# Kernel tuning notes

Measured on AMD Instinct MI355X. Metric: run time of the kernel, lower is better.

The kernel has to match this reference:

```python
import jax, jax.numpy as jnp
import numpy as np
import math

# ---- irreps config: (multiplicity, l); parity implied by the fixed path list ----
IRREPS_IN = [(32, 0), (32, 1)]    # "32x0e + 32x1o" -> dim 128
IRREPS_SH = [(1, 0), (1, 1), (1, 2)]  # "1x0e + 1x1o + 1x2e" -> dim 9
IRREPS_OUT = [(32, 0), (32, 1)]   # dim 128
# parity/triangle-allowed 'uvw' instructions: (in_block, sh_block, out_block)
PATHS = [(0, 0, 0), (0, 1, 1), (1, 0, 1), (1, 1, 0), (1, 2, 1)]
NUM_NODES = 50000
NUM_EDGES = 800000


def _fact(n):
    return math.factorial(int(round(n)))


def _su2_cg(j1, j2, j3):
    """SU(2) Clebsch-Gordan coefficients via the Racah formula."""
    C = np.zeros((2 * j1 + 1, 2 * j2 + 1, 2 * j3 + 1))
    for m1 in range(-j1, j1 + 1):
        for m2 in range(-j2, j2 + 1):
            m3 = m1 + m2
            if abs(m3) > j3:
                continue
            vmin = int(max(-j1 + j2 + m3, -j1 + m1, 0))
            vmax = int(min(j2 + j3 + m1, j3 - j1 + j2, j3 + m3))
            c = math.sqrt((2 * j3 + 1) * _fact(j3 + j1 - j2) * _fact(j3 - j1 + j2)
                          * _fact(j1 + j2 - j3) / _fact(j1 + j2 + j3 + 1))
            c *= math.sqrt(_fact(j3 + m3) * _fact(j3 - m3) * _fact(j1 - m1)
                           * _fact(j1 + m1) * _fact(j2 - m2) * _fact(j2 + m2))
            s = 0.0
            for v in range(vmin, vmax + 1):
                s += ((-1.0) ** (v + j2 + m2) * _fact(j2 + j3 + m1 - v) * _fact(j1 - m1 + v)
                      / (_fact(v) * _fact(j3 - j1 + j2 - v) * _fact(j3 + m3 - v) * _fact(v + j1 - j2 - m3)))
            C[j1 + m1, j2 + m2, j3 + m3] = c * s
    return C


def _q(l):
    """Change of basis real -> complex spherical harmonics (e3nn convention)."""
    q = np.zeros((2 * l + 1, 2 * l + 1), dtype=np.complex128)
    for m in range(-l, 0):
        q[l + m, l + abs(m)] = 1.0 / np.sqrt(2.0)
        q[l + m, l - abs(m)] = -1j / np.sqrt(2.0)
    q[l, l] = 1.0
    for m in range(1, l + 1):
        q[l + m, l + abs(m)] = (-1.0) ** m / np.sqrt(2.0)
        q[l + m, l - abs(m)] = 1j * (-1.0) ** m / np.sqrt(2.0)
    return (-1j) ** l * q


def _real_cg(l1, l2, l3):
    """Real (Wigner-3j-like) Clebsch-Gordan tensor, unit Frobenius norm."""
    C = _su2_cg(l1, l2, l3).astype(np.complex128)
    C = np.einsum('ij,kl,mn,ikn->jlm', _q(l1), _q(l2), np.conj(_q(l3).T), C)
    C = np.real(C)
    return (C / np.linalg.norm(C)).astype(np.float32)


CG = [jnp.asarray(_real_cg(IRREPS_IN[i1][1], IRREPS_SH[i2][1], IRREPS_OUT[io][1]))
      for (i1, i2, io) in PATHS]
N_PATHS_TO_OUT = {io: sum(1 for p in PATHS if p[2] == io) for io in range(len(IRREPS_OUT))}


def _split(x, irreps):
    """Split flat irreps vector into [E, mul, 2l+1] blocks."""
    blocks, off = [], 0
    for mul, l in irreps:
        d = mul * (2 * l + 1)
        blocks.append(x[:, off:off + d].reshape(x.shape[0], mul, 2 * l + 1))
        off += d
    return blocks


def setup_inputs() -> dict:
    key = jax.random.key(0)
    k1, k2, k3, k4 = jax.random.split(key, 4)
    in_dim = sum(m * (2 * l + 1) for m, l in IRREPS_IN)
    sh_dim = sum(m * (2 * l + 1) for m, l in IRREPS_SH)
    features = jax.random.normal(k1, (NUM_NODES, in_dim), dtype=jnp.float32)
    edge_sh = jax.random.normal(k2, (NUM_EDGES, sh_dim), dtype=jnp.float32)
    edge_index = jax.random.randint(k3, (2, NUM_EDGES), 0, NUM_NODES, dtype=jnp.int32)
    # shared 'uvw' weights: one [mul_in=32, mul_out=32] matrix per path (mul_sh=1)
    weights = jax.random.normal(k4, (len(PATHS), 32, 32), dtype=jnp.float32)
    return {"features": features, "edge_sh": edge_sh,
            "edge_index": edge_index, "weights": weights}


def reference(features, edge_sh, edge_index, weights):
    src, dst = edge_index[0], edge_index[1]
    x1 = _split(features[src], IRREPS_IN)   # gather source node features per edge
    x2 = _split(edge_sh, IRREPS_SH)
    out_blocks = [None] * len(IRREPS_OUT)
    for p, (i1, i2, io) in enumerate(PATHS):
        u, v = IRREPS_IN[i1][0], IRREPS_SH[i2][0]
        alpha = 1.0 / math.sqrt(u * v * N_PATHS_TO_OUT[io])
        # tmp: [E, u, 2*l3+1]; sh block has mul 1 -> squeeze
        tmp = jnp.einsum('eui,ej,ijk->euk', x1[i1], x2[i2][:, 0, :], CG[p])
        msg = jnp.einsum('euk,uw->ewk', tmp, weights[p]) * alpha
        out_blocks[io] = msg if out_blocks[io] is None else out_blocks[io] + msg
    E = edge_sh.shape[0]
    msgs = jnp.concatenate([b.reshape(E, -1) for b in out_blocks], axis=1)  # [E, 128]
    out = jnp.zeros((features.shape[0], msgs.shape[1]), dtype=features.dtype)
    return out.at[dst].add(msgs)  # scatter-add to destination nodes
```

## Files before the change

### kernel.cpp

```cpp
#include <hip/hip_runtime.h>
#include <math.h>


typedef __attribute__((ext_vector_type(8))) short bf16x8;
typedef __attribute__((ext_vector_type(4))) float f32x4;

__device__ inline float blo(unsigned u) { return __uint_as_float(u << 16); }
__device__ inline float bhi(unsigned u) { return __uint_as_float(u & 0xffff0000u); }
__device__ inline unsigned bpack(float a, float b) {
    unsigned ua = __float_as_uint(a);
    ua = (ua + 0x7fffu + ((ua >> 16) & 1u)) >> 16;
    unsigned ub = __float_as_uint(b);
    ub = (ub + 0x7fffu + ((ub >> 16) & 1u)) & 0xffff0000u;
    return ua | ub;
}
__device__ inline unsigned short bh(float a) {
    unsigned ua = __float_as_uint(a);
    return (unsigned short)((ua + 0x7fffu + ((ua >> 16) & 1u)) >> 16);
}

__device__ inline float dfactf(int n) {
    float r = 1.0f;
    for (int i = 2; i <= n; ++i) r *= (float)i;
    return r;
}

__device__ float su2_cg_elem_f(int l1, int l2, int l3, int i, int k, int n) {
    int m1 = i - l1, m2 = k - l2, m3 = n - l3;
    if (m1 + m2 != m3) return 0.0f;
    int vmin = -l1 + l2 + m3;
    if (-l1 + m1 > vmin) vmin = -l1 + m1;
    if (0 > vmin) vmin = 0;
    int vmax = l2 + l3 + m1;
    if (l3 - l1 + l2 < vmax) vmax = l3 - l1 + l2;
    if (l3 + m3 < vmax) vmax = l3 + m3;
    if (vmax < vmin) return 0.0f;
    float c = sqrtf((float)(2 * l3 + 1) * dfactf(l3 + l1 - l2) *
                    dfactf(l3 - l1 + l2) * dfactf(l1 + l2 - l3) /
                    dfactf(l1 + l2 + l3 + 1));
    c *= sqrtf(dfactf(l3 + m3) * dfactf(l3 - m3) * dfactf(l1 - m1) *
               dfactf(l1 + m1) * dfactf(l2 - m2) * dfactf(l2 + m2));
    float s = 0.0f;
    for (int v = vmin; v <= vmax; ++v) {
        float term = dfactf(l2 + l3 + m1 - v) * dfactf(l1 - m1 + v) /
                     (dfactf(v) * dfactf(l3 - l1 + l2 - v) *
                      dfactf(l3 + m3 - v) * dfactf(v + l1 - l2 - m3));
        if ((v + l2 + m2) & 1) term = -term;
        s += term;
    }
    return c * s;
}

__device__ void cg_compute_block(float* __restrict__ cg_out) {
    __shared__ float sqr[3][5][5], sqi[3][5][5];
    __shared__ float vals[5][45];
    int t = threadIdx.x;
    if (t < 75) {
        int l = t / 25, a = (t % 25) / 5, b = t % 5;
        float re = 0.f, im = 0.f;
        const float inv = 0.70710678118654752440f;
        int m = a - l;
        if (a < 5 && b < 5) {
            if (m < 0) {
                if (b == l - m) re = inv;
                if (b == l + m) im = -inv;
            } else if (m == 0) {
                if (b == l && a == l) re = 1.f;
            } else {
                float sgn = (m & 1) ? -1.f : 1.f;
                if (b == l + m) re = sgn * inv;
                if (b == l - m) im = sgn * inv;
            }
        }
        if (l == 1) { float r = re; re = im; im = -r; }
        else if (l == 2) { re = -re; im = -im; }
        sqr[l][a][b] = re;
        sqi[l][a][b] = im;
    }
    __syncthreads();
    const int l1s[5] = {0, 0, 1, 1, 1};
    const int l2s[5] = {0, 1, 0, 1, 2};
    const int l3s[5] = {0, 1, 1, 0, 1};
    const int offs[5] = {0, 1, 10, 19, 28};
    const float alphas[5] = {0.125f, 0.10206207261596575f, 0.10206207261596575f,
                             0.125f, 0.10206207261596575f};
    int p = t / 45, idx = t % 45;
    bool active = (t < 225);
    float acc = 0.0f;
    int d1 = 0, d2 = 0, d3 = 0;
    int l1 = 0, l2 = 0, l3 = 0;
    if (active) {
        l1 = l1s[p]; l2 = l2s[p]; l3 = l3s[p];
        d1 = 2 * l1 + 1; d2 = 2 * l2 + 1; d3 = 2 * l3 + 1;
        if (idx < d1 * d2 * d3) {
            int j = idx / (d2 * d3);
            int rem = idx % (d2 * d3);
            int l_ = rem / d3, m = rem % d3;
            for (int i = 0; i < d1; ++i)
                for (int k = 0; k < d2; ++k)
                    for (int n = 0; n < d3; ++n) {
                        float C = su2_cg_elem_f(l1, l2, l3, i, k, n);
                        if (C == 0.0f) continue;
                        float ar = sqr[l1][i][j], ai = sqi[l1][i][j];
                        float br = sqr[l2][k][l_], bi = sqi[l2][k][l_];
                        float cr = sqr[l3][n][m], ci = sqi[l3][n][m];
                        float abr = ar * br - ai * bi;
                        float abi = ar * bi + ai * br;
                        acc += (abr * cr + abi * ci) * C;
                    }
        }
        vals[p][idx] = acc;
    }
    __syncthreads();
    if (active && idx < d1 * d2 * d3) {
        float n2 = 0.0f;
        for (int q = 0; q < 45; ++q) n2 += vals[p][q] * vals[p][q];
        cg_out[offs[p] + idx] = acc * alphas[p] / sqrtf(n2);
    }
}

__global__ __launch_bounds__(256) void prep_kernel(
    const float* __restrict__ feat, const int* __restrict__ eidx,
    int* __restrict__ cursor, unsigned* __restrict__ fb,
    float* __restrict__ cg, int N, int E) {
    if (blockIdx.x == 0) cg_compute_block(cg);
    int t = blockIdx.x * 256 + threadIdx.x;
    if (t < N * 32) {
        int n = t >> 5, u = t & 31;
        const float* f = feat + (size_t)n * 128;
        float s = f[u];
        float vx = f[32 + 3 * u], vy = f[33 + 3 * u], vz = f[34 + 3 * u];
        ((uint2*)fb)[t] = make_uint2(bpack(s, vx), bpack(vy, vz));
    }
    if (t < E) atomicAdd(&cursor[eidx[E + t]], 1);
}

__global__ __launch_bounds__(256) void scanA_kernel(
    const int* __restrict__ counts, int* __restrict__ tilesums, int N,
    const float* __restrict__ W, const float* __restrict__ cg,
    unsigned short* __restrict__ WBT) {
    __shared__ int lds[4];
    int i = blockIdx.x * 256 + threadIdx.x;
    int v = (i < N) ? counts[i] : 0;
#pragma unroll
    for (int d = 1; d < 64; d <<= 1) v += __shfl_xor(v, d);
    int wid = threadIdx.x >> 6;
    if ((threadIdx.x & 63) == 0) lds[wid] = v;
    __syncthreads();
    if (threadIdx.x == 0)
        tilesums[blockIdx.x] = lds[0] + lds[1] + lds[2] + lds[3];
    int idx = i;
    if (idx < 128 * 352) {
        int j = idx / 352, k = idx % 352;
        int t = k >> 5, u = k & 31;
        float val = 0.f;
        if (j < 32) {
            if (t == 0) val = cg[0] * W[u * 32 + j];
            else if (t == 1) val = W[3072 + u * 32 + j];
        } else {
            int w = (j - 32) / 3, m = (j - 32) % 3;
            if (t >= 2 && t <= 4) { if (t - 2 == m) val = W[1024 + u * 32 + w]; }
            else if (t >= 5 && t <= 7) { val = cg[10 + (t - 5) * 3 + m] * W[2048 + u * 32 + w]; }
            else if (t >= 8) { if (t - 8 == m) val = W[4096 + u * 32 + w]; }
        }
        WBT[idx] = bh(val);
    }
}

__global__ __launch_bounds__(256) void scanB_kernel(
    int* __restrict__ tilesums, int tiles) {
    __shared__ int lds[4];
    int tid = threadIdx.x;
    int v = (tid < tiles) ? tilesums[tid] : 0;
    int orig = v;
#pragma unroll
    for (int d = 1; d < 64; d <<= 1) {
        int t = __shfl_up(v, d);
        if ((tid & 63) >= d) v += t;
    }
    int wid = tid >> 6;
    if ((tid & 63) == 63) lds[wid] = v;
    __syncthreads();
    int base = 0;
    for (int q = 0; q < wid; ++q) base += lds[q];
    if (tid < tiles) tilesums[tid] = base + v - orig;
}

__global__ __launch_bounds__(256) void scanC_kernel(
    int* __restrict__ counts, const int* __restrict__ tilesums, int N) {
    __shared__ int lds[4];
    int i = blockIdx.x * 256 + threadIdx.x;
    int tid = threadIdx.x;
    int v = (i < N) ? counts[i] : 0;
    int orig = v;
#pragma unroll
    for (int d = 1; d < 64; d <<= 1) {
        int t = __shfl_up(v, d);
        if ((tid & 63) >= d) v += t;
    }
    int wid = tid >> 6;
    if ((tid & 63) == 63) lds[wid] = v;
    __syncthreads();
    int base = tilesums[blockIdx.x];
    for (int q = 0; q < wid; ++q) base += lds[q];
    if (i < N) counts[i] = base + v - orig;
}

__global__ __launch_bounds__(256) void zscatter_kernel(
    const int* __restrict__ eidx, const float* __restrict__ sh,
    const float* __restrict__ cg, int* __restrict__ cursor,
    unsigned* __restrict__ zrec, int E) {
    int t = blockIdx.x * 256 + threadIdx.x;
    if (t >= E) return;
    int src = eidx[t];
    int dst = eidx[E + t];
    int pos = atomicAdd(&cursor[dst], 1);
    const float* Ye = sh + (size_t)t * 9;
    float Y0 = Ye[0];
    float Y1v[3] = {Ye[1], Ye[2], Ye[3]};
    float Y2v[5] = {Ye[4], Ye[5], Ye[6], Ye[7], Ye[8]};
    float Z1[3], Z3[3], Z4[9];
#pragma unroll
    for (int m = 0; m < 3; ++m)
        Z1[m] = fmaf(Y1v[0], cg[1 + m],
                fmaf(Y1v[1], cg[4 + m], Y1v[2] * cg[7 + m]));
#pragma unroll
    for (int i = 0; i < 3; ++i)
        Z3[i] = fmaf(Y1v[0], cg[19 + i * 3],
                fmaf(Y1v[1], cg[19 + i * 3 + 1], Y1v[2] * cg[19 + i * 3 + 2]));
#pragma unroll
    for (int i = 0; i < 3; ++i)
#pragma unroll
        for (int m = 0; m < 3; ++m) {
            float acc = 0.f;
#pragma unroll
            for (int j = 0; j < 5; ++j)
                acc = fmaf(Y2v[j], cg[28 + (i * 5 + j) * 3 + m], acc);
            Z4[i * 3 + m] = acc;
        }
    uint2* rec = (uint2*)(zrec + (size_t)pos * 10);
    rec[0] = make_uint2((unsigned)src, bpack(Y0, Z1[0]));
    rec[1] = make_uint2(bpack(Z1[1], Z1[2]), bpack(Z3[0], Z3[1]));
    rec[2] = make_uint2(bpack(Z3[2], Z4[0]), bpack(Z4[1], Z4[2]));
    rec[3] = make_uint2(bpack(Z4[3], Z4[4]), bpack(Z4[5], Z4[6]));
    rec[4] = make_uint2(bpack(Z4[7], Z4[8]), 0u);
}

__global__ __launch_bounds__(256) void gather_kernel(
    const unsigned* __restrict__ fb, const unsigned* __restrict__ zrec,
    const int* __restrict__ cursor, unsigned short* __restrict__ G, int N) {
    int wave = (blockIdx.x * 256 + threadIdx.x) >> 6;
    int lane = threadIdx.x & 63;
    if (wave >= N) return;
    int start = wave ? cursor[wave - 1] : 0;
    int end = cursor[wave];
    int half = lane >> 5, u = lane & 31;

    float g0 = 0.f, g3 = 0.f;
    float g1x = 0.f, g1y = 0.f, g1z = 0.f;
    float g2x = 0.f, g2y = 0.f, g2z = 0.f;
    float g4x = 0.f, g4y = 0.f, g4z = 0.f;

    for (int idx = start + half; idx < end; idx += 2) {
        const uint2* r = (const uint2*)(zrec + (size_t)idx * 10);
        uint2 r0 = r[0], r1 = r[1], r2 = r[2], r3 = r[3], r4 = r[4];
        int src = (int)r0.x;
        uint2 f2 = ((const uint2*)fb)[(size_t)src * 32 + u];
        float s = blo(f2.x), vx = bhi(f2.x);
        float vy = blo(f2.y), vz = bhi(f2.y);
        float y0 = blo(r0.y), z10 = bhi(r0.y);
        float z11 = blo(r1.x), z12 = bhi(r1.x);
        float z30 = blo(r1.y), z31 = bhi(r1.y);
        float z32 = blo(r2.x), z400 = bhi(r2.x);
        float z401 = blo(r2.y), z402 = bhi(r2.y);
        float z410 = blo(r3.x), z411 = bhi(r3.x);
        float z412 = blo(r3.y), z420 = bhi(r3.y);
        float z421 = blo(r4.x), z422 = bhi(r4.x);

        g0 = fmaf(y0, s, g0);
        g1x = fmaf(z10, s, g1x); g1y = fmaf(z11, s, g1y); g1z = fmaf(z12, s, g1z);
        g2x = fmaf(y0, vx, g2x); g2y = fmaf(y0, vy, g2y); g2z = fmaf(y0, vz, g2z);
        g3 = fmaf(z30, vx, fmaf(z31, vy, fmaf(z32, vz, g3)));
        g4x = fmaf(vx, z400, fmaf(vy, z410, fmaf(vz, z420, g4x)));
        g4y = fmaf(vx, z401, fmaf(vy, z411, fmaf(vz, z421, g4y)));
        g4z = fmaf(vx, z402, fmaf(vy, z412, fmaf(vz, z422, g4z)));
    }
    g0 += __shfl_xor(g0, 32);  g3 += __shfl_xor(g3, 32);
    g1x += __shfl_xor(g1x, 32); g1y += __shfl_xor(g1y, 32); g1z += __shfl_xor(g1z, 32);
    g2x += __shfl_xor(g2x, 32); g2y += __shfl_xor(g2y, 32); g2z += __shfl_xor(g2z, 32);
    g4x += __shfl_xor(g4x, 32); g4y += __shfl_xor(g4y, 32); g4z += __shfl_xor(g4z, 32);

    if (half == 0) {
        unsigned short* Gr = G + (size_t)wave * 352 + u;
        Gr[0] = bh(g0);
        Gr[32] = bh(g3);
        Gr[64] = bh(g1x);  Gr[96] = bh(g1y);  Gr[128] = bh(g1z);
        Gr[160] = bh(g2x); Gr[192] = bh(g2y); Gr[224] = bh(g2z);
        Gr[256] = bh(g4x); Gr[288] = bh(g4y); Gr[320] = bh(g4z);
    }
}

__global__ __launch_bounds__(256) void epilogue_kernel(
    const unsigned short* __restrict__ G, const unsigned short* __restrict__ WBT,
    float* __restrict__ out, int N) {
    int wid = (blockIdx.x * 256 + threadIdx.x) >> 6;
    int lane = threadIdx.x & 63;
    int ntiles = N >> 4;
    if (wid >= ntiles) return;
    int n0 = wid << 4;
    int r = lane & 15, q = lane >> 4;

    bf16x8 a[11];
#pragma unroll
    for (int kk = 0; kk < 11; ++kk)
        a[kk] = *(const bf16x8*)(G + (size_t)(n0 + r) * 352 + kk * 32 + q * 8);

#pragma unroll
    for (int jt = 0; jt < 8; ++jt) {
        f32x4 acc = {0.f, 0.f, 0.f, 0.f};
#pragma unroll
        for (int kk = 0; kk < 11; ++kk) {
            bf16x8 b = *(const bf16x8*)(WBT + (size_t)(jt * 16 + r) * 352 + kk * 32 + q * 8);
            acc = __builtin_amdgcn_mfma_f32_16x16x32_bf16(a[kk], b, acc, 0, 0, 0);
        }
#pragma unroll
        for (int i = 0; i < 4; ++i)
            out[(size_t)(n0 + q * 4 + i) * 128 + jt * 16 + r] = acc[i];
    }
}

extern "C" void kernel_launch(void* const* d_in, const int* in_sizes, int n_in,
                              void* d_out, int out_size, void* d_ws, size_t ws_size,
                              hipStream_t stream) {
    const float* feat = (const float*)d_in[0];
    const float* sh = (const float*)d_in[1];
    const int* eidx = (const int*)d_in[2];
    const float* W = (const float*)d_in[3];
    float* out = (float*)d_out;
    int N = in_sizes[0] / 128;
    int E = in_sizes[1] / 9;

    float* wsf = (float*)d_ws;
    float* cg = wsf;
    int* cursor = (int*)(wsf + 128);
    size_t off = (size_t)(128 + N + 1) & ~(size_t)1;
    unsigned* zrec = (unsigned*)(wsf + off);
    unsigned* fb = zrec + (size_t)10 * E;
    unsigned short* G = (unsigned short*)(fb + (size_t)64 * N);
    unsigned short* WBT = G + (size_t)352 * N;
    int* tilesums = (int*)(WBT + 45056);

    int tiles = (N + 255) / 256;

    hipMemsetAsync(cursor, 0, (size_t)N * sizeof(int), stream);
    prep_kernel<<<(N * 32 + 255) / 256, 256, 0, stream>>>(feat, eidx, cursor, fb, cg, N, E);
    scanA_kernel<<<tiles, 256, 0, stream>>>(cursor, tilesums, N, W, cg, WBT);
    scanB_kernel<<<1, 256, 0, stream>>>(tilesums, tiles);
    scanC_kernel<<<tiles, 256, 0, stream>>>(cursor, tilesums, N);
    zscatter_kernel<<<(E + 255) / 256, 256, 0, stream>>>(eidx, sh, cg, cursor, zrec, E);
    gather_kernel<<<(N * 64 + 255) / 256, 256, 0, stream>>>(fb, zrec, cursor, G, N);
    epilogue_kernel<<<((N >> 4) * 64 + 255) / 256, 256, 0, stream>>>(G, WBT, out, N);
}
```

Baseline: 186.0 us.

## Fuse gather and MFMA epilogue kernels via shared-memory G tile

Merges the per-node gather kernel and the MFMA epilogue into one kernel. Each block gathers 16 nodes, four per wave, into a shared-memory bf16 tile, then runs the 16x352x128 MFMA product, with each wave producing two of the eight output column tiles. This removes the global round trip of the G buffer and one kernel launch. In exchange each wave processes four nodes serially and there is a block-wide barrier, which cuts parallelism and latency hiding in the gather phase.

```diff
diff --git a/kernel.cpp b/kernel.cpp
--- a/kernel.cpp
+++ b/kernel.cpp
@@ -88,9 +88,8 @@
     bool active = (t < 225);
     float acc = 0.0f;
     int d1 = 0, d2 = 0, d3 = 0;
-    int l1 = 0, l2 = 0, l3 = 0;
     if (active) {
-        l1 = l1s[p]; l2 = l2s[p]; l3 = l3s[p];
+        int l1 = l1s[p], l2 = l2s[p], l3 = l3s[p];
         d1 = 2 * l1 + 1; d2 = 2 * l2 + 1; d3 = 2 * l3 + 1;
         if (idx < d1 * d2 * d3) {
             int j = idx / (d2 * d3);
@@ -246,77 +245,78 @@
     rec[4] = make_uint2(bpack(Z4[7], Z4[8]), 0u);
 }
 
-__global__ __launch_bounds__(256) void gather_kernel(
+__global__ __launch_bounds__(256) void gather_mfma_kernel(
     const unsigned* __restrict__ fb, const unsigned* __restrict__ zrec,
-    const int* __restrict__ cursor, unsigned short* __restrict__ G, int N) {
-    int wave = (blockIdx.x * 256 + threadIdx.x) >> 6;
+    const int* __restrict__ cursor, const unsigned short* __restrict__ WBT,
+    float* __restrict__ out, int N) {
+    __shared__ unsigned short Gs[16][360];
+    int wv = threadIdx.x >> 6;
     int lane = threadIdx.x & 63;
-    if (wave >= N) return;
-    int start = wave ? cursor[wave - 1] : 0;
-    int end = cursor[wave];
     int half = lane >> 5, u = lane & 31;
-
-    float g0 = 0.f, g3 = 0.f;
-    float g1x = 0.f, g1y = 0.f, g1z = 0.f;
-    float g2x = 0.f, g2y = 0.f, g2z = 0.f;
-    float g4x = 0.f, g4y = 0.f, g4z = 0.f;
-
-    for (int idx = start + half; idx < end; idx += 2) {
-        const uint2* r = (const uint2*)(zrec + (size_t)idx * 10);
-        uint2 r0 = r[0], r1 = r[1], r2 = r[2], r3 = r[3], r4 = r[4];
-        int src = (int)r0.x;
-        uint2 f2 = ((const uint2*)fb)[(size_t)src * 32 + u];
-        float s = blo(f2.x), vx = bhi(f2.x);
-        float vy = blo(f2.y), vz = bhi(f2.y);
-        float y0 = blo(r0.y), z10 = bhi(r0.y);
-        float z11 = blo(r1.x), z12 = bhi(r1.x);
-        float z30 = blo(r1.y), z31 = bhi(r1.y);
-        float z32 = blo(r2.x), z400 = bhi(r2.x);
-        float z401 = blo(r2.y), z402 = bhi(r2.y);
-        float z410 = blo(r3.x), z411 = bhi(r3.x);
-        float z412 = blo(r3.y), z420 = bhi(r3.y);
-        float z421 = blo(r4.x), z422 = bhi(r4.x);
-
-        g0 = fmaf(y0, s, g0);
-        g1x = fmaf(z10, s, g1x); g1y = fmaf(z11, s, g1y); g1z = fmaf(z12, s, g1z);
-        g2x = fmaf(y0, vx, g2x); g2y = fmaf(y0, vy, g2y); g2z = fmaf(y0, vz, g2z);
-        g3 = fmaf(z30, vx, fmaf(z31, vy, fmaf(z32, vz, g3)));
-        g4x = fmaf(vx, z400, fmaf(vy, z410, fmaf(vz, z420, g4x)));
-        g4y = fmaf(vx, z401, fmaf(vy, z411, fmaf(vz, z421, g4y)));
-        g4z = fmaf(vx, z402, fmaf(vy, z412, fmaf(vz, z422, g4z)));
-    }
-    g0 += __shfl_xor(g0, 32);  g3 += __shfl_xor(g3, 32);
-    g1x += __shfl_xor(g1x, 32); g1y += __shfl_xor(g1y, 32); g1z += __shfl_xor(g1z, 32);
-    g2x += __shfl_xor(g2x, 32); g2y += __shfl_xor(g2y, 32); g2z += __shfl_xor(g2z, 32);
-    g4x += __shfl_xor(g4x, 32); g4y += __shfl_xor(g4y, 32); g4z += __shfl_xor(g4z, 32);
-
-    if (half == 0) {
-        unsigned short* Gr = G + (size_t)wave * 352 + u;
-        Gr[0] = bh(g0);
-        Gr[32] = bh(g3);
-        Gr[64] = bh(g1x);  Gr[96] = bh(g1y);  Gr[128] = bh(g1z);
-        Gr[160] = bh(g2x); Gr[192] = bh(g2y); Gr[224] = bh(g2z);
-        Gr[256] = bh(g4x); Gr[288] = bh(g4y); Gr[320] = bh(g4z);
-    }
-}
-
-__global__ __launch_bounds__(256) void epilogue_kernel(
-    const unsigned short* __restrict__ G, const unsigned short* __restrict__ WBT,
-    float* __restrict__ out, int N) {
-    int wid = (blockIdx.x * 256 + threadIdx.x) >> 6;
-    int lane = threadIdx.x & 63;
-    int ntiles = N >> 4;
-    if (wid >= ntiles) return;
-    int n0 = wid << 4;
+    int base = blockIdx.x << 4;
+
+#pragma unroll 1
+    for (int d = 0; d < 4; ++d) {
+        int row = wv * 4 + d;
+        int node = base + row;
+        if (node >= N) break;
+        int start = node ? cursor[node - 1] : 0;
+        int end = cursor[node];
+
+        float g0 = 0.f, g3 = 0.f;
+        float g1x = 0.f, g1y = 0.f, g1z = 0.f;
+        float g2x = 0.f, g2y = 0.f, g2z = 0.f;
+        float g4x = 0.f, g4y = 0.f, g4z = 0.f;
+
+        for (int idx = start + half; idx < end; idx += 2) {
+            const uint2* r = (const uint2*)(zrec + (size_t)idx * 10);
+            uint2 r0 = r[0], r1 = r[1], r2 = r[2], r3 = r[3], r4 = r[4];
+            int src = (int)r0.x;
+            uint2 f2 = ((const uint2*)fb)[(size_t)src * 32 + u];
+            float s = blo(f2.x), vx = bhi(f2.x);
+            float vy = blo(f2.y), vz = bhi(f2.y);
+            float y0 = blo(r0.y), z10 = bhi(r0.y);
+            float z11 = blo(r1.x), z12 = bhi(r1.x);
+            float z30 = blo(r1.y), z31 = bhi(r1.y);
+            float z32 = blo(r2.x), z400 = bhi(r2.x);
+            float z401 = blo(r2.y), z402 = bhi(r2.y);
+            float z410 = blo(r3.x), z411 = bhi(r3.x);
+            float z412 = blo(r3.y), z420 = bhi(r3.y);
+            float z421 = blo(r4.x), z422 = bhi(r4.x);
+
+            g0 = fmaf(y0, s, g0);
+            g1x = fmaf(z10, s, g1x); g1y = fmaf(z11, s, g1y); g1z = fmaf(z12, s, g1z);
+            g2x = fmaf(y0, vx, g2x); g2y = fmaf(y0, vy, g2y); g2z = fmaf(y0, vz, g2z);
+            g3 = fmaf(z30, vx, fmaf(z31, vy, fmaf(z32, vz, g3)));
+            g4x = fmaf(vx, z400, fmaf(vy, z410, fmaf(vz, z420, g4x)));
+            g4y = fmaf(vx, z401, fmaf(vy, z411, fmaf(vz, z421, g4y)));
+            g4z = fmaf(vx, z402, fmaf(vy, z412, fmaf(vz, z422, g4z)));
+        }
+        g0 += __shfl_xor(g0, 32);  g3 += __shfl_xor(g3, 32);
+        g1x += __shfl_xor(g1x, 32); g1y += __shfl_xor(g1y, 32); g1z += __shfl_xor(g1z, 32);
+        g2x += __shfl_xor(g2x, 32); g2y += __shfl_xor(g2y, 32); g2z += __shfl_xor(g2z, 32);
+        g4x += __shfl_xor(g4x, 32); g4y += __shfl_xor(g4y, 32); g4z += __shfl_xor(g4z, 32);
+
+        if (half == 0) {
+            unsigned short* Gr = &Gs[row][u];
+            Gr[0] = bh(g0);
+            Gr[32] = bh(g3);
+            Gr[64] = bh(g1x);  Gr[96] = bh(g1y);  Gr[128] = bh(g1z);
+            Gr[160] = bh(g2x); Gr[192] = bh(g2y); Gr[224] = bh(g2z);
+            Gr[256] = bh(g4x); Gr[288] = bh(g4y); Gr[320] = bh(g4z);
+        }
+    }
+    __syncthreads();
+
     int r = lane & 15, q = lane >> 4;
-
     bf16x8 a[11];
 #pragma unroll
     for (int kk = 0; kk < 11; ++kk)
-        a[kk] = *(const bf16x8*)(G + (size_t)(n0 + r) * 352 + kk * 32 + q * 8);
-
-#pragma unroll
-    for (int jt = 0; jt < 8; ++jt) {
+        a[kk] = *(const bf16x8*)(&Gs[r][kk * 32 + q * 8]);
+
+#pragma unroll
+    for (int jj = 0; jj < 2; ++jj) {
+        int jt = wv * 2 + jj;
         f32x4 acc = {0.f, 0.f, 0.f, 0.f};
 #pragma unroll
         for (int kk = 0; kk < 11; ++kk) {
@@ -324,8 +324,10 @@
             acc = __builtin_amdgcn_mfma_f32_16x16x32_bf16(a[kk], b, acc, 0, 0, 0);
         }
 #pragma unroll
-        for (int i = 0; i < 4; ++i)
-            out[(size_t)(n0 + q * 4 + i) * 128 + jt * 16 + r] = acc[i];
+        for (int i = 0; i < 4; ++i) {
+            int n = base + q * 4 + i;
+            if (n < N) out[(size_t)n * 128 + jt * 16 + r] = acc[i];
+        }
     }
 }
 
@@ -346,11 +348,11 @@
     size_t off = (size_t)(128 + N + 1) & ~(size_t)1;
     unsigned* zrec = (unsigned*)(wsf + off);
     unsigned* fb = zrec + (size_t)10 * E;
-    unsigned short* G = (unsigned short*)(fb + (size_t)64 * N);
-    unsigned short* WBT = G + (size_t)352 * N;
+    unsigned short* WBT = (unsigned short*)(fb + (size_t)64 * N);
     int* tilesums = (int*)(WBT + 45056);
 
     int tiles = (N + 255) / 256;
+    int ntiles16 = (N + 15) / 16;
 
     hipMemsetAsync(cursor, 0, (size_t)N * sizeof(int), stream);
     prep_kernel<<<(N * 32 + 255) / 256, 256, 0, stream>>>(feat, eidx, cursor, fb, cg, N, E);
@@ -358,6 +360,5 @@
     scanB_kernel<<<1, 256, 0, stream>>>(tilesums, tiles);
     scanC_kernel<<<tiles, 256, 0, stream>>>(cursor, tilesums, N);
     zscatter_kernel<<<(E + 255) / 256, 256, 0, stream>>>(eidx, sh, cg, cursor, zrec, E);
-    gather_kernel<<<(N * 64 + 255) / 256, 256, 0, stream>>>(fb, zrec, cursor, G, N);
-    epilogue_kernel<<<((N >> 4) * 64 + 255) / 256, 256, 0, stream>>>(G, WBT, out, N);
-}
+    gather_mfma_kernel<<<ntiles16, 256, 0, stream>>>(fb, zrec, cursor, WBT, out, N);
+}
```

After: 179.5 us. -3.5%, faster.
